# Kernel tuning notes

Hardware: AMD Instinct MI355X
Metric: run time of the kernel (lower is better)

The kernel has to match this reference:

```python
import jax, jax.numpy as jnp
import numpy as np

N_NODES = 50000
N_EDGES = 640000
D = 128
N_RELS = 16
N_NTYPES = 8


def setup_inputs() -> dict:
    key = jax.random.key(0)
    ks = jax.random.split(key, 9)
    return {
        "feats": jax.random.normal(ks[0], (N_NODES, D), dtype=jnp.float32),
        "W_edge": jax.random.normal(ks[1], (N_RELS, D, D), dtype=jnp.float32) / np.sqrt(D),
        "b_edge": jax.random.normal(ks[2], (N_RELS, D), dtype=jnp.float32) * 0.02,
        "W_node": jax.random.normal(ks[3], (N_NTYPES, D, D), dtype=jnp.float32) / np.sqrt(D),
        "b_node": jax.random.normal(ks[4], (N_NTYPES, D), dtype=jnp.float32) * 0.02,
        "src": jax.random.randint(ks[5], (N_EDGES,), 0, N_NODES, dtype=jnp.int32),
        "dst": jax.random.randint(ks[6], (N_EDGES,), 0, N_NODES, dtype=jnp.int32),
        "ntypes": jax.random.randint(ks[7], (N_NODES,), 0, N_NTYPES, dtype=jnp.int32),
        "etypes": jax.random.randint(ks[8], (N_EDGES,), 0, N_RELS, dtype=jnp.int32),
    }


def reference(feats, W_edge, b_edge, W_node, b_node, src, dst, ntypes, etypes):
    N, d = feats.shape
    T = W_edge.shape[0]
    # Per-relation linear applied to all nodes once: [T, N, out]; then gather per edge.
    hW = jnp.einsum('nd,tdf->tnf', feats, W_edge) + b_edge[:, None, :]
    msg = hW[etypes, src]  # [E, out]
    # Per-(dst-node, edge-type) in-degree counts (one_hot count normalization).
    seg = dst * T + etypes  # [E]
    counts = jax.ops.segment_sum(jnp.ones(msg.shape[0], dtype=msg.dtype), seg,
                                 num_segments=N * T)  # [N*T]
    msg = msg / counts[seg][:, None]
    # Scatter-sum messages into destination nodes (zero for isolated nodes).
    agg = jax.ops.segment_sum(msg, dst, num_segments=N)  # [N, out]
    # Type-conditional node transform + residual message + activation.
    hN = jnp.einsum('nd,tdf->tnf', feats, W_node) + b_node[:, None, :]  # [Tn, N, out]
    out = hN[ntypes, jnp.arange(N)] + agg
    return jax.nn.relu(out)
```

## Files before the change

kernel.cpp:

```cpp
#include <hip/hip_runtime.h>
#include <hip/hip_bf16.h>
#include <stdint.h>


#define D 128
#define TRELS 16
#define NTYPES 8

typedef __bf16 bf16x8 __attribute__((ext_vector_type(8)));
typedef float f32x4 __attribute__((ext_vector_type(4)));
typedef unsigned int u32x4 __attribute__((ext_vector_type(4)));

__device__ __forceinline__ unsigned short f2bf(float f) {
  union { float f; unsigned u; } v; v.f = f;
  unsigned u = v.u;
  return (unsigned short)((u + 0x7FFFu + ((u >> 16) & 1u)) >> 16);
}
__device__ __forceinline__ float bf2f(unsigned short h) {
  union { unsigned u; float f; } v; v.u = ((unsigned)h) << 16;
  return v.f;
}
__device__ __forceinline__ void bfpair(unsigned u, float& lo, float& hi) {
  union { unsigned u; float f; } a, b;
  a.u = u << 16; b.u = u & 0xffff0000u;
  lo = a.f; hi = b.f;
}

__global__ void prep_k(const float* __restrict__ feats,
                       const float* __restrict__ We,
                       const float* __restrict__ Wn,
                       unsigned short* __restrict__ featsbf,
                       unsigned short* __restrict__ WeT,
                       unsigned short* __restrict__ WnT,
                       int nfeat) {
  int idx = blockIdx.x * 256 + threadIdx.x;
  if (idx < nfeat) { featsbf[idx] = f2bf(feats[idx]); return; }
  idx -= nfeat;
  if (idx < TRELS * D * D) {
    int t = idx >> 14, rem = idx & 16383;
    int n = rem >> 7, k = rem & 127;
    WeT[idx] = f2bf(We[t * 16384 + k * 128 + n]);
    return;
  }
  idx -= TRELS * D * D;
  if (idx < NTYPES * D * D) {
    int t = idx >> 14, rem = idx & 16383;
    int n = rem >> 7, k = rem & 127;
    WnT[idx] = f2bf(Wn[t * 16384 + k * 128 + n]);
  }
}

__global__ void hist_k(const int* __restrict__ dst, const int* __restrict__ etypes,
                       const int* __restrict__ ntypes, int E, int N,
                       int* __restrict__ cnt, int* __restrict__ nhist) {
  __shared__ int sh_n[NTYPES];
  int tid = threadIdx.x;
  if (tid < NTYPES) sh_n[tid] = 0;
  __syncthreads();
  int g = blockIdx.x * 256 + tid;
  if (g < E) atomicAdd(&cnt[dst[g] * TRELS + etypes[g]], 1);
  if (g < N) atomicAdd(&sh_n[ntypes[g]], 1);
  __syncthreads();
  if (tid < NTYPES && sh_n[tid]) atomicAdd(&nhist[tid], sh_n[tid]);
}

__global__ void scan1_k(const int* __restrict__ cnt, int* __restrict__ doff,
                        int* __restrict__ bsum, int N) {
  __shared__ int sd[256];
  int b = blockIdx.x, tid = threadIdx.x;
  int base = b * 1024 + tid * 4;
  int v[4]; int tot = 0;
  for (int j = 0; j < 4; ++j) {
    int i = base + j;
    int dg = 0;
    if (i < N) {
      const int* row = cnt + i * TRELS;
#pragma unroll
      for (int et = 0; et < TRELS; ++et) dg += row[et];
    }
    v[j] = tot; tot += dg;
  }
  sd[tid] = tot;
  __syncthreads();
  for (int off = 1; off < 256; off <<= 1) {
    int t = (tid >= off) ? sd[tid - off] : 0;
    __syncthreads();
    sd[tid] += t;
    __syncthreads();
  }
  int excl = sd[tid] - tot;
  for (int j = 0; j < 4; ++j) {
    int i = base + j;
    if (i < N) doff[i] = excl + v[j];
  }
  if (tid == 255) bsum[b] = sd[255];
}

__global__ void scan2_k(int* __restrict__ misc, int* __restrict__ bsum, int nb) {
  if (threadIdx.x != 0) return;
  int run = 0;
  for (int b = 0; b < nb; ++b) { int t = bsum[b]; bsum[b] = run; run += t; }
  int* noff = misc; int* ntb = misc + 9; int* ncur = misc + 18; int* nhist = misc + 26;
  int s = 0, ts = 0;
  for (int t = 0; t < NTYPES; ++t) {
    noff[t] = s; ncur[t] = s; ntb[t] = ts;
    s += nhist[t]; ts += (nhist[t] + 127) >> 7;
  }
  noff[NTYPES] = s; ntb[NTYPES] = ts;
}

__global__ void scan3_k(int* __restrict__ doff, int* __restrict__ dcur,
                        const int* __restrict__ bsum, int N, int E) {
  int b = blockIdx.x, tid = threadIdx.x;
  int add = bsum[b];
  int base = b * 1024 + tid * 4;
  for (int j = 0; j < 4; ++j) {
    int i = base + j;
    if (i < N) { int o = doff[i] + add; doff[i] = o; dcur[i] = o; }
  }
  if (b == 0 && tid == 0) doff[N] = E;
}

__global__ void scatter_k(const int* __restrict__ src, const int* __restrict__ dst,
                          const int* __restrict__ etypes, const int* __restrict__ ntypes,
                          int E, int N, int* __restrict__ misc,
                          int* __restrict__ dcur,
                          int* __restrict__ edst, int* __restrict__ nsorted) {
  __shared__ int lc_n[NTYPES], lb_n[NTYPES];
  int tid = threadIdx.x;
  if (tid < NTYPES) lc_n[tid] = 0;
  __syncthreads();
  int g = blockIdx.x * 256 + tid;
  if (g < E) {
    int d = dst[g];
    int pos = atomicAdd(&dcur[d], 1);
    edst[pos] = src[g] * TRELS + etypes[g];
  }
  int tn = -1, idn = 0;
  if (g < N) { tn = ntypes[g]; idn = atomicAdd(&lc_n[tn], 1); }
  __syncthreads();
  if (tid < NTYPES && lc_n[tid]) lb_n[tid] = atomicAdd(&misc[18 + tid], lc_n[tid]);
  __syncthreads();
  if (g < N) nsorted[lb_n[tn] + idn] = g;
}

__global__ __launch_bounds__(256) void hw_gemm_k(
    const unsigned short* __restrict__ featsbf,
    const unsigned short* __restrict__ WeT,
    unsigned short* __restrict__ hW, int N, int mtiles) {
  __shared__ unsigned char Asm[128 * 264];
  int tid = threadIdx.x;

  int G = mtiles * 16;
  int q = G >> 3, rmod = G & 7;
  int xcd = blockIdx.x & 7, bidx = blockIdx.x >> 3;
  int wrk = (xcd < rmod) ? (xcd * (q + 1) + bidx)
                         : (rmod * (q + 1) + (xcd - rmod) * q + bidx);
  int tile = wrk >> 4;
  int et = wrk & 15;

  int lane = tid & 63, w = tid >> 6;
  int m = lane & 15, qd = lane >> 4;
  int rw = (w & 1) * 64, cw = (w >> 1) * 64;

  const unsigned short* WB = WeT + et * (D * D);
  bf16x8 bfr[4][4];
#pragma unroll
  for (int ks = 0; ks < 4; ++ks)
#pragma unroll
    for (int j = 0; j < 4; ++j)
      bfr[ks][j] = *reinterpret_cast<const bf16x8*>(WB + (cw + j * 16 + m) * D + ks * 32 + qd * 8);

  int r = tid >> 1, h = tid & 1;
  int row = tile * 128 + r;
  if (row < N) {
    const u32x4* gp = reinterpret_cast<const u32x4*>(featsbf + (size_t)row * D);
#pragma unroll
    for (int cc = 0; cc < 8; ++cc) {
      int c = h * 8 + cc;
      *reinterpret_cast<u32x4*>(&Asm[r * 256 + ((c ^ (r & 7)) << 4)]) = gp[c];
    }
  }
  __syncthreads();

  f32x4 acc[4][4];
#pragma unroll
  for (int i = 0; i < 4; ++i)
#pragma unroll
    for (int j = 0; j < 4; ++j) acc[i][j] = (f32x4){0.f, 0.f, 0.f, 0.f};

#pragma unroll
  for (int ks = 0; ks < 4; ++ks) {
    bf16x8 a[4];
#pragma unroll
    for (int i = 0; i < 4; ++i) {
      int rr = rw + i * 16 + m;
      int c = ks * 4 + qd;
      a[i] = *reinterpret_cast<const bf16x8*>(&Asm[rr * 256 + ((c ^ (rr & 7)) << 4)]);
    }
#pragma unroll
    for (int i = 0; i < 4; ++i)
#pragma unroll
      for (int j = 0; j < 4; ++j)
        acc[i][j] = __builtin_amdgcn_mfma_f32_16x16x32_bf16(a[i], bfr[ks][j], acc[i][j], 0, 0, 0);
  }

  __syncthreads();
  unsigned short* Cs = reinterpret_cast<unsigned short*>(Asm);
#pragma unroll
  for (int i = 0; i < 4; ++i)
#pragma unroll
    for (int j = 0; j < 4; ++j)
#pragma unroll
      for (int reg = 0; reg < 4; ++reg) {
        int rr = rw + i * 16 + qd * 4 + reg;
        Cs[rr * 132 + cw + j * 16 + m] = f2bf(acc[i][j][reg]);
      }
  __syncthreads();
  char* gout = (char*)(hW + ((size_t)et * N + (size_t)tile * 128) * D);
#pragma unroll
  for (int cp = 0; cp < 8; ++cp) {
    int o = cp * 4096 + tid * 16;
    int rloc = o >> 8;
    if (tile * 128 + rloc < N) {
      u32x4 v = *reinterpret_cast<const u32x4*>(&Asm[rloc * 264 + (o & 255)]);
      __builtin_nontemporal_store(v, reinterpret_cast<u32x4*>(gout + o));
    }
  }
}

__global__ __launch_bounds__(256) void agg_k(
    const unsigned short* __restrict__ hW,
    const float* __restrict__ b_edge,
    const int* __restrict__ cnt,
    const int* __restrict__ doff, const int* __restrict__ edst,
    float* __restrict__ agg, int N) {
  int tid = threadIdx.x;
  int lane = tid & 63, w = tid >> 6;
  int d = blockIdx.x * 4 + w;
  if (d >= N) return;

  int cv = 0;
  if (lane < TRELS) cv = cnt[d * TRELS + lane];
  float invl = (cv > 0) ? 1.0f / (float)cv : 0.0f;

  int g = lane >> 4;
  int sub = lane & 15;

  int start = doff[d], end = doff[d + 1];
  float acc[8];
#pragma unroll
  for (int z = 0; z < 8; ++z) acc[z] = 0.f;

  for (int base = start; base < end; base += 64) {
    int key = 0;
    if (base + lane < end) key = edst[base + lane];
    int nchunk = end - base; if (nchunk > 64) nchunk = 64;
#pragma unroll 2
    for (int j = 0; j < nchunk; j += 4) {
      int rr = j + g;
      int k = __shfl(key, rr, 64);
      float inv = __shfl(invl, k & 15, 64);
      if (rr < nchunk) {
        const unsigned short* hp =
            hW + ((size_t)(k & 15) * N + (size_t)(k >> 4)) * D + sub * 8;
        u32x4 hv = *reinterpret_cast<const u32x4*>(hp);
        float lo, hi;
        bfpair(hv.x, lo, hi); acc[0] += inv * lo; acc[1] += inv * hi;
        bfpair(hv.y, lo, hi); acc[2] += inv * lo; acc[3] += inv * hi;
        bfpair(hv.z, lo, hi); acc[4] += inv * lo; acc[5] += inv * hi;
        bfpair(hv.w, lo, hi); acc[6] += inv * lo; acc[7] += inv * hi;
      }
    }
  }

#pragma unroll
  for (int z = 0; z < 8; ++z) {
    acc[z] += __shfl_xor(acc[z], 16, 64);
    acc[z] += __shfl_xor(acc[z], 32, 64);
  }

  int cb = sub * 8 + (g & 1) * 4;
  f32x4 res = { acc[(g & 1) * 4 + 0], acc[(g & 1) * 4 + 1],
                acc[(g & 1) * 4 + 2], acc[(g & 1) * 4 + 3] };
#pragma unroll
  for (int et = 0; et < TRELS; ++et) {
    int c = __shfl(cv, et, 64);
    if (c > 0) {
      f32x4 b4 = *reinterpret_cast<const f32x4*>(b_edge + et * D + cb);
#pragma unroll
      for (int z = 0; z < 4; ++z) res[z] += b4[z];
    }
  }
  if (g < 2)
    *reinterpret_cast<f32x4*>(agg + (size_t)d * D + cb) = res;
}

__global__ __launch_bounds__(256) void node_gemm_k(
    const unsigned short* __restrict__ featsbf,
    const unsigned short* __restrict__ WnT,
    const float* __restrict__ b_node,
    const int* __restrict__ nsorted, const int* __restrict__ misc,
    const float* __restrict__ agg,
    float* __restrict__ out) {
  __shared__ unsigned char Asm[128 * 264];
  __shared__ int sm_node[128];
  __shared__ int s_ntb[9];
  int tid = threadIdx.x;
  if (tid < 9) s_ntb[tid] = misc[9 + tid];
  __syncthreads();
  int bid = blockIdx.x;
  if (bid >= s_ntb[8]) return;
  int t = 0;
  while (bid >= s_ntb[t + 1]) ++t;
  int tile = bid - s_ntb[t];
  int noff_t = misc[t];
  int cntT = misc[t + 1] - noff_t;

  int lane = tid & 63, w = tid >> 6;
  int m = lane & 15, q = lane >> 4;
  int rw = (w & 1) * 64, cw = (w >> 1) * 64;

  const unsigned short* WB = WnT + t * (D * D);
  bf16x8 bfr[4][4];
#pragma unroll
  for (int ks = 0; ks < 4; ++ks)
#pragma unroll
    for (int j = 0; j < 4; ++j)
      bfr[ks][j] = *reinterpret_cast<const bf16x8*>(WB + (cw + j * 16 + m) * D + ks * 32 + q * 8);

  int r = tid >> 1, h = tid & 1;
  int gidx = tile * 128 + r;
  bool rv = gidx < cntT;
  int node = 0;
  if (rv) node = nsorted[noff_t + gidx];
  if (h == 0) sm_node[r] = rv ? node : -1;
  if (rv) {
    const u32x4* gp = reinterpret_cast<const u32x4*>(featsbf + (size_t)node * D);
#pragma unroll
    for (int cc = 0; cc < 8; ++cc) {
      int c = h * 8 + cc;
      *reinterpret_cast<u32x4*>(&Asm[r * 256 + ((c ^ (r & 7)) << 4)]) = gp[c];
    }
  }
  __syncthreads();

  f32x4 acc[4][4];
#pragma unroll
  for (int i = 0; i < 4; ++i)
#pragma unroll
    for (int j = 0; j < 4; ++j) acc[i][j] = (f32x4){0.f, 0.f, 0.f, 0.f};

#pragma unroll
  for (int ks = 0; ks < 4; ++ks) {
    bf16x8 a[4];
#pragma unroll
    for (int i = 0; i < 4; ++i) {
      int rr = rw + i * 16 + m;
      int c = ks * 4 + q;
      a[i] = *reinterpret_cast<const bf16x8*>(&Asm[rr * 256 + ((c ^ (rr & 7)) << 4)]);
    }
#pragma unroll
    for (int i = 0; i < 4; ++i)
#pragma unroll
      for (int j = 0; j < 4; ++j)
        acc[i][j] = __builtin_amdgcn_mfma_f32_16x16x32_bf16(a[i], bfr[ks][j], acc[i][j], 0, 0, 0);
  }

  const float* bnp = b_node + t * D;
  float* Cf = reinterpret_cast<float*>(Asm);
  __syncthreads();
#pragma unroll
  for (int half = 0; half < 2; ++half) {
    if ((w & 1) == half) {
#pragma unroll
      for (int i = 0; i < 4; ++i)
#pragma unroll
        for (int j = 0; j < 4; ++j)
#pragma unroll
          for (int reg = 0; reg < 4; ++reg) {
            int rl = i * 16 + q * 4 + reg;
            Cf[rl * 132 + cw + j * 16 + m] = acc[i][j][reg];
          }
    }
    __syncthreads();
#pragma unroll
    for (int cp = 0; cp < 8; ++cp) {
      int o = cp * 4096 + tid * 16;
      int rl = o >> 9;
      int nd = sm_node[half * 64 + rl];
      if (nd >= 0) {
        int col = (o & 511) >> 2;
        f32x4 c = *reinterpret_cast<const f32x4*>((char*)Cf + rl * 528 + (o & 511));
        f32x4 a = *reinterpret_cast<const f32x4*>(agg + (size_t)nd * D + col);
        f32x4 b4 = *reinterpret_cast<const f32x4*>(bnp + col);
        f32x4 res;
#pragma unroll
        for (int z = 0; z < 4; ++z) res[z] = fmaxf(c[z] + a[z] + b4[z], 0.f);
        *reinterpret_cast<f32x4*>(out + (size_t)nd * D + col) = res;
      }
    }
    __syncthreads();
  }
}

static inline size_t align256(size_t x) { return (x + 255) & ~(size_t)255; }

extern "C" void kernel_launch(void* const* d_in, const int* in_sizes, int n_in,
                              void* d_out, int out_size, void* d_ws, size_t ws_size,
                              hipStream_t stream) {
  const float* feats  = (const float*)d_in[0];
  const float* W_edge = (const float*)d_in[1];
  const float* b_edge = (const float*)d_in[2];
  const float* W_node = (const float*)d_in[3];
  const float* b_node = (const float*)d_in[4];
  const int* src    = (const int*)d_in[5];
  const int* dst    = (const int*)d_in[6];
  const int* ntypes = (const int*)d_in[7];
  const int* etypes = (const int*)d_in[8];
  int N = in_sizes[0] / D;
  int E = in_sizes[5];

  char* ws = (char*)d_ws;
  size_t o_cnt  = 0;
  size_t o_misc = align256(o_cnt + (size_t)N * TRELS * 4);
  size_t zend   = align256(o_misc + 512);
  size_t o_doff = zend;
  size_t o_dcur = align256(o_doff + (size_t)(N + 1) * 4);
  size_t o_edst = align256(o_dcur + (size_t)N * 4);
  size_t o_ns   = align256(o_edst + (size_t)E * 4);
  size_t o_fb   = align256(o_ns + (size_t)N * 4);
  size_t o_we   = align256(o_fb + (size_t)N * D * 2);
  size_t o_wn   = align256(o_we + (size_t)TRELS * D * D * 2);
  size_t o_agg  = align256(o_wn + (size_t)NTYPES * D * D * 2);
  size_t o_hw   = align256(o_agg + (size_t)N * D * 4);

  int* cnt = (int*)(ws + o_cnt);
  int* misc = (int*)(ws + o_misc);
  int* doff = (int*)(ws + o_doff);
  int* dcur = (int*)(ws + o_dcur);
  int* edst = (int*)(ws + o_edst);
  int* nsorted = (int*)(ws + o_ns);
  unsigned short* featsbf = (unsigned short*)(ws + o_fb);
  unsigned short* WeT = (unsigned short*)(ws + o_we);
  unsigned short* WnT = (unsigned short*)(ws + o_wn);
  float* agg = (float*)(ws + o_agg);
  unsigned short* hW = (unsigned short*)(ws + o_hw);
  int* bsum = misc + 64;

  (void)hipMemsetAsync(ws, 0, zend, stream);

  int nfeat = N * D;
  int ptot = nfeat + TRELS * D * D + NTYPES * D * D;
  prep_k<<<(ptot + 255) / 256, 256, 0, stream>>>(feats, W_edge, W_node, featsbf, WeT, WnT, nfeat);

  int hgrid = ((E > N ? E : N) + 255) / 256;
  hist_k<<<hgrid, 256, 0, stream>>>(dst, etypes, ntypes, E, N, cnt, misc + 26);

  int nb = (N + 1023) / 1024;
  scan1_k<<<nb, 256, 0, stream>>>(cnt, doff, bsum, N);
  scan2_k<<<1, 64, 0, stream>>>(misc, bsum, nb);
  scan3_k<<<nb, 256, 0, stream>>>(doff, dcur, bsum, N, E);

  scatter_k<<<hgrid, 256, 0, stream>>>(src, dst, etypes, ntypes, E, N, misc, dcur, edst, nsorted);

  int mtiles = (N + 127) / 128;
  hw_gemm_k<<<mtiles * 16, 256, 0, stream>>>(featsbf, WeT, hW, N, mtiles);

  agg_k<<<(N + 3) / 4, 256, 0, stream>>>(hW, b_edge, cnt, doff, edst, agg, N);

  int ngrid = mtiles + NTYPES;
  node_gemm_k<<<ngrid, 256, 0, stream>>>(featsbf, WnT, b_node, nsorted, misc, agg, (float*)d_out);
}
```

Before: 347.4 us.

## Reuse staged feature tile across four relations per block in hW GEMM

Each hW GEMM block now loads its 128-row feature tile into LDS once and computes four relation outputs, so the grid shrinks by four and A-tile reloads are amortised. The next relation's weights are prefetched into registers while the current output is written back through a separate 64-row LDS staging buffer in two halves, and a launch bound of 3 blocks per SM is added. Nontemporal stores become plain stores. In exchange there are more barriers per block, higher register pressure, and fewer blocks to spread across the GPU.

New measurement: 359.3 us. 3.4% more time.

```diff
diff --git a/kernel.cpp b/kernel.cpp
--- a/kernel.cpp
+++ b/kernel.cpp
@@ -6,6 +6,7 @@
 #define D 128
 #define TRELS 16
 #define NTYPES 8
+#define ETC 4
 
 typedef __bf16 bf16x8 __attribute__((ext_vector_type(8)));
 typedef float f32x4 __attribute__((ext_vector_type(4)));
@@ -144,32 +145,25 @@
   if (g < N) nsorted[lb_n[tn] + idn] = g;
 }
 
-__global__ __launch_bounds__(256) void hw_gemm_k(
+__global__ __launch_bounds__(256, 3) void hw_gemm_k(
     const unsigned short* __restrict__ featsbf,
     const unsigned short* __restrict__ WeT,
     unsigned short* __restrict__ hW, int N, int mtiles) {
   __shared__ unsigned char Asm[128 * 264];
+  __shared__ unsigned char Csm[64 * 264];
   int tid = threadIdx.x;
 
-  int G = mtiles * 16;
+  int G = mtiles * (TRELS / ETC);
   int q = G >> 3, rmod = G & 7;
   int xcd = blockIdx.x & 7, bidx = blockIdx.x >> 3;
   int wrk = (xcd < rmod) ? (xcd * (q + 1) + bidx)
                          : (rmod * (q + 1) + (xcd - rmod) * q + bidx);
-  int tile = wrk >> 4;
-  int et = wrk & 15;
+  int tile = wrk >> 2;
+  int etbase = (wrk & 3) * ETC;
 
   int lane = tid & 63, w = tid >> 6;
   int m = lane & 15, qd = lane >> 4;
   int rw = (w & 1) * 64, cw = (w >> 1) * 64;
-
-  const unsigned short* WB = WeT + et * (D * D);
-  bf16x8 bfr[4][4];
-#pragma unroll
-  for (int ks = 0; ks < 4; ++ks)
-#pragma unroll
-    for (int j = 0; j < 4; ++j)
-      bfr[ks][j] = *reinterpret_cast<const bf16x8*>(WB + (cw + j * 16 + m) * D + ks * 32 + qd * 8);
 
   int r = tid >> 1, h = tid & 1;
   int row = tile * 128 + r;
@@ -181,50 +175,79 @@
       *reinterpret_cast<u32x4*>(&Asm[r * 256 + ((c ^ (r & 7)) << 4)]) = gp[c];
     }
   }
-  __syncthreads();
-
-  f32x4 acc[4][4];
-#pragma unroll
-  for (int i = 0; i < 4; ++i)
-#pragma unroll
-    for (int j = 0; j < 4; ++j) acc[i][j] = (f32x4){0.f, 0.f, 0.f, 0.f};
-
-#pragma unroll
-  for (int ks = 0; ks < 4; ++ks) {
-    bf16x8 a[4];
-#pragma unroll
-    for (int i = 0; i < 4; ++i) {
-      int rr = rw + i * 16 + m;
-      int c = ks * 4 + qd;
-      a[i] = *reinterpret_cast<const bf16x8*>(&Asm[rr * 256 + ((c ^ (rr & 7)) << 4)]);
-    }
+
+  bf16x8 bfr[4][4];
+  {
+    const unsigned short* WB = WeT + (size_t)etbase * (D * D);
+#pragma unroll
+    for (int ks = 0; ks < 4; ++ks)
+#pragma unroll
+      for (int j = 0; j < 4; ++j)
+        bfr[ks][j] = *reinterpret_cast<const bf16x8*>(WB + (cw + j * 16 + m) * D + ks * 32 + qd * 8);
+  }
+  __syncthreads();
+
+#pragma unroll
+  for (int e = 0; e < ETC; ++e) {
+    int et = etbase + e;
+
+    f32x4 acc[4][4];
 #pragma unroll
     for (int i = 0; i < 4; ++i)
 #pragma unroll
-      for (int j = 0; j < 4; ++j)
-        acc[i][j] = __builtin_amdgcn_mfma_f32_16x16x32_bf16(a[i], bfr[ks][j], acc[i][j], 0, 0, 0);
-  }
-
-  __syncthreads();
-  unsigned short* Cs = reinterpret_cast<unsigned short*>(Asm);
-#pragma unroll
-  for (int i = 0; i < 4; ++i)
-#pragma unroll
-    for (int j = 0; j < 4; ++j)
-#pragma unroll
-      for (int reg = 0; reg < 4; ++reg) {
-        int rr = rw + i * 16 + qd * 4 + reg;
-        Cs[rr * 132 + cw + j * 16 + m] = f2bf(acc[i][j][reg]);
+      for (int j = 0; j < 4; ++j) acc[i][j] = (f32x4){0.f, 0.f, 0.f, 0.f};
+
+#pragma unroll
+    for (int ks = 0; ks < 4; ++ks) {
+      bf16x8 a[4];
+#pragma unroll
+      for (int i = 0; i < 4; ++i) {
+        int rr = rw + i * 16 + m;
+        int c = ks * 4 + qd;
+        a[i] = *reinterpret_cast<const bf16x8*>(&Asm[rr * 256 + ((c ^ (rr & 7)) << 4)]);
       }
-  __syncthreads();
-  char* gout = (char*)(hW + ((size_t)et * N + (size_t)tile * 128) * D);
-#pragma unroll
-  for (int cp = 0; cp < 8; ++cp) {
-    int o = cp * 4096 + tid * 16;
-    int rloc = o >> 8;
-    if (tile * 128 + rloc < N) {
-      u32x4 v = *reinterpret_cast<const u32x4*>(&Asm[rloc * 264 + (o & 255)]);
-      __builtin_nontemporal_store(v, reinterpret_cast<u32x4*>(gout + o));
+#pragma unroll
+      for (int i = 0; i < 4; ++i)
+#pragma unroll
+        for (int j = 0; j < 4; ++j)
+          acc[i][j] = __builtin_amdgcn_mfma_f32_16x16x32_bf16(a[i], bfr[ks][j], acc[i][j], 0, 0, 0);
+    }
+
+    if (e + 1 < ETC) {
+      const unsigned short* WB = WeT + (size_t)(et + 1) * (D * D);
+#pragma unroll
+      for (int ks = 0; ks < 4; ++ks)
+#pragma unroll
+        for (int j = 0; j < 4; ++j)
+          bfr[ks][j] = *reinterpret_cast<const bf16x8*>(WB + (cw + j * 16 + m) * D + ks * 32 + qd * 8);
+    }
+
+    char* gout = (char*)(hW + ((size_t)et * N + (size_t)tile * 128) * D);
+    unsigned short* Cs = reinterpret_cast<unsigned short*>(Csm);
+#pragma unroll
+    for (int half = 0; half < 2; ++half) {
+      __syncthreads();
+      if ((w & 1) == half) {
+#pragma unroll
+        for (int i = 0; i < 4; ++i)
+#pragma unroll
+          for (int j = 0; j < 4; ++j)
+#pragma unroll
+            for (int reg = 0; reg < 4; ++reg) {
+              int rl = i * 16 + qd * 4 + reg;
+              Cs[rl * 132 + cw + j * 16 + m] = f2bf(acc[i][j][reg]);
+            }
+      }
+      __syncthreads();
+#pragma unroll
+      for (int cp = 0; cp < 4; ++cp) {
+        int o = cp * 4096 + tid * 16;
+        int rloc = o >> 8;
+        if (tile * 128 + half * 64 + rloc < N) {
+          u32x4 v = *reinterpret_cast<const u32x4*>(&Csm[rloc * 264 + (o & 255)]);
+          *reinterpret_cast<u32x4*>(gout + half * 16384 + o) = v;
+        }
+      }
     }
   }
 }
@@ -465,7 +488,7 @@
   scatter_k<<<hgrid, 256, 0, stream>>>(src, dst, etypes, ntypes, E, N, misc, dcur, edst, nsorted);
 
   int mtiles = (N + 127) / 128;
-  hw_gemm_k<<<mtiles * 16, 256, 0, stream>>>(featsbf, WeT, hW, N, mtiles);
+  hw_gemm_k<<<mtiles * (TRELS / ETC), 256, 0, stream>>>(featsbf, WeT, hW, N, mtiles);
 
   agg_k<<<(N + 3) / 4, 256, 0, stream>>>(hW, b_edge, cnt, doff, edst, agg, N);
 
```

## Split edge-relation GEMM and aggregation into two half-relation passes for cache residency

Applied to the files above, without the earlier changes.

Splits the per-relation transform into two passes of 8 relations each, with each pass writing a half-size hW buffer (about 100MB bf16 instead of 200MB) and then running aggregation over only the edges of those relations. The second aggregation pass adds its result into agg. Stores are switched from nontemporal to regular so the half buffer can stay resident in the large last-level cache for the gather. The cost is two extra launches, a second pass over the edge lists and a read-modify-write of agg.

Measured after the change: 367.0 us. 1.06x slower.

```diff
diff --git a/kernel.cpp b/kernel.cpp
--- a/kernel.cpp
+++ b/kernel.cpp
@@ -6,6 +6,7 @@
 #define D 128
 #define TRELS 16
 #define NTYPES 8
+#define ETPH 8
 
 typedef __bf16 bf16x8 __attribute__((ext_vector_type(8)));
 typedef float f32x4 __attribute__((ext_vector_type(4)));
@@ -147,23 +148,23 @@
 __global__ __launch_bounds__(256) void hw_gemm_k(
     const unsigned short* __restrict__ featsbf,
     const unsigned short* __restrict__ WeT,
-    unsigned short* __restrict__ hW, int N, int mtiles) {
+    unsigned short* __restrict__ hWp, int N, int mtiles, int etoff) {
   __shared__ unsigned char Asm[128 * 264];
   int tid = threadIdx.x;
 
-  int G = mtiles * 16;
+  int G = mtiles * ETPH;
   int q = G >> 3, rmod = G & 7;
   int xcd = blockIdx.x & 7, bidx = blockIdx.x >> 3;
   int wrk = (xcd < rmod) ? (xcd * (q + 1) + bidx)
                          : (rmod * (q + 1) + (xcd - rmod) * q + bidx);
-  int tile = wrk >> 4;
-  int et = wrk & 15;
+  int tile = wrk >> 3;
+  int etl = wrk & 7;
 
   int lane = tid & 63, w = tid >> 6;
   int m = lane & 15, qd = lane >> 4;
   int rw = (w & 1) * 64, cw = (w >> 1) * 64;
 
-  const unsigned short* WB = WeT + et * (D * D);
+  const unsigned short* WB = WeT + (size_t)(etoff + etl) * (D * D);
   bf16x8 bfr[4][4];
 #pragma unroll
   for (int ks = 0; ks < 4; ++ks)
@@ -217,24 +218,24 @@
         Cs[rr * 132 + cw + j * 16 + m] = f2bf(acc[i][j][reg]);
       }
   __syncthreads();
-  char* gout = (char*)(hW + ((size_t)et * N + (size_t)tile * 128) * D);
+  char* gout = (char*)(hWp + ((size_t)etl * N + (size_t)tile * 128) * D);
 #pragma unroll
   for (int cp = 0; cp < 8; ++cp) {
     int o = cp * 4096 + tid * 16;
     int rloc = o >> 8;
     if (tile * 128 + rloc < N) {
       u32x4 v = *reinterpret_cast<const u32x4*>(&Asm[rloc * 264 + (o & 255)]);
-      __builtin_nontemporal_store(v, reinterpret_cast<u32x4*>(gout + o));
+      *reinterpret_cast<u32x4*>(gout + o) = v;
     }
   }
 }
 
 __global__ __launch_bounds__(256) void agg_k(
-    const unsigned short* __restrict__ hW,
+    const unsigned short* __restrict__ hWp,
     const float* __restrict__ b_edge,
     const int* __restrict__ cnt,
     const int* __restrict__ doff, const int* __restrict__ edst,
-    float* __restrict__ agg, int N) {
+    float* __restrict__ agg, int N, int etoff, int pass) {
   int tid = threadIdx.x;
   int lane = tid & 63, w = tid >> 6;
   int d = blockIdx.x * 4 + w;
@@ -261,9 +262,10 @@
       int rr = j + g;
       int k = __shfl(key, rr, 64);
       float inv = __shfl(invl, k & 15, 64);
-      if (rr < nchunk) {
+      unsigned etl = (unsigned)((k & 15) - etoff);
+      if (rr < nchunk && etl < (unsigned)ETPH) {
         const unsigned short* hp =
-            hW + ((size_t)(k & 15) * N + (size_t)(k >> 4)) * D + sub * 8;
+            hWp + ((size_t)etl * N + (size_t)(k >> 4)) * D + sub * 8;
         u32x4 hv = *reinterpret_cast<const u32x4*>(hp);
         float lo, hi;
         bfpair(hv.x, lo, hi); acc[0] += inv * lo; acc[1] += inv * hi;
@@ -283,17 +285,26 @@
   int cb = sub * 8 + (g & 1) * 4;
   f32x4 res = { acc[(g & 1) * 4 + 0], acc[(g & 1) * 4 + 1],
                 acc[(g & 1) * 4 + 2], acc[(g & 1) * 4 + 3] };
-#pragma unroll
-  for (int et = 0; et < TRELS; ++et) {
-    int c = __shfl(cv, et, 64);
-    if (c > 0) {
-      f32x4 b4 = *reinterpret_cast<const f32x4*>(b_edge + et * D + cb);
-#pragma unroll
-      for (int z = 0; z < 4; ++z) res[z] += b4[z];
-    }
-  }
-  if (g < 2)
-    *reinterpret_cast<f32x4*>(agg + (size_t)d * D + cb) = res;
+  if (pass == 0) {
+#pragma unroll
+    for (int et = 0; et < TRELS; ++et) {
+      int c = __shfl(cv, et, 64);
+      if (c > 0) {
+        f32x4 b4 = *reinterpret_cast<const f32x4*>(b_edge + et * D + cb);
+#pragma unroll
+        for (int z = 0; z < 4; ++z) res[z] += b4[z];
+      }
+    }
+  }
+  if (g < 2) {
+    f32x4* op = reinterpret_cast<f32x4*>(agg + (size_t)d * D + cb);
+    if (pass) {
+      f32x4 old = *op;
+#pragma unroll
+      for (int z = 0; z < 4; ++z) res[z] += old[z];
+    }
+    *op = res;
+  }
 }
 
 __global__ __launch_bounds__(256) void node_gemm_k(
@@ -465,9 +476,11 @@
   scatter_k<<<hgrid, 256, 0, stream>>>(src, dst, etypes, ntypes, E, N, misc, dcur, edst, nsorted);
 
   int mtiles = (N + 127) / 128;
-  hw_gemm_k<<<mtiles * 16, 256, 0, stream>>>(featsbf, WeT, hW, N, mtiles);
-
-  agg_k<<<(N + 3) / 4, 256, 0, stream>>>(hW, b_edge, cnt, doff, edst, agg, N);
+  int agrid = (N + 3) / 4;
+  hw_gemm_k<<<mtiles * ETPH, 256, 0, stream>>>(featsbf, WeT, hW, N, mtiles, 0);
+  agg_k<<<agrid, 256, 0, stream>>>(hW, b_edge, cnt, doff, edst, agg, N, 0, 0);
+  hw_gemm_k<<<mtiles * ETPH, 256, 0, stream>>>(featsbf, WeT, hW, N, mtiles, 8);
+  agg_k<<<agrid, 256, 0, stream>>>(hW, b_edge, cnt, doff, edst, agg, N, 8, 1);
 
   int ngrid = mtiles + NTYPES;
   node_gemm_k<<<ngrid, 256, 0, stream>>>(featsbf, WnT, b_node, nsorted, misc, agg, (float*)d_out);
```

## Fuse per-relation aggregation before transform, eliminating the hW intermediate

Applied to the files above, without the earlier changes.

Sorts edges by (dst, relation) bucket and, per 64-destination tile, averages raw bf16 source features per relation, then multiplies by each relation's weight with MFMA and accumulates. Bias is added once per nonempty relation. This avoids materialising and re-reading the large per-relation transformed feature tensor. In exchange, the scan grows to N×16 entries, and the fused kernel serialises edge gathers per thread with many block barriers. Precision also changes, since averaged features are rounded to bf16 before the GEMM.

Measured after the change: 462.0 us. +33.0%, slower.

```diff
diff --git a/kernel.cpp b/kernel.cpp
--- a/kernel.cpp
+++ b/kernel.cpp
@@ -6,6 +6,7 @@
 #define D 128
 #define TRELS 16
 #define NTYPES 8
+#define DSTB 64
 
 typedef __bf16 bf16x8 __attribute__((ext_vector_type(8)));
 typedef float f32x4 __attribute__((ext_vector_type(4)));
@@ -15,10 +16,6 @@
   union { float f; unsigned u; } v; v.f = f;
   unsigned u = v.u;
   return (unsigned short)((u + 0x7FFFu + ((u >> 16) & 1u)) >> 16);
-}
-__device__ __forceinline__ float bf2f(unsigned short h) {
-  union { unsigned u; float f; } v; v.u = ((unsigned)h) << 16;
-  return v.f;
 }
 __device__ __forceinline__ void bfpair(unsigned u, float& lo, float& hi) {
   union { unsigned u; float f; } a, b;
@@ -64,21 +61,16 @@
   if (tid < NTYPES && sh_n[tid]) atomicAdd(&nhist[tid], sh_n[tid]);
 }
 
-__global__ void scan1_k(const int* __restrict__ cnt, int* __restrict__ doff,
-                        int* __restrict__ bsum, int N) {
+__global__ void scan1_k(const int* __restrict__ cnt, int* __restrict__ poff,
+                        int* __restrict__ bsum, int M) {
   __shared__ int sd[256];
   int b = blockIdx.x, tid = threadIdx.x;
   int base = b * 1024 + tid * 4;
   int v[4]; int tot = 0;
   for (int j = 0; j < 4; ++j) {
     int i = base + j;
-    int dg = 0;
-    if (i < N) {
-      const int* row = cnt + i * TRELS;
-#pragma unroll
-      for (int et = 0; et < TRELS; ++et) dg += row[et];
-    }
-    v[j] = tot; tot += dg;
+    int c = (i < M) ? cnt[i] : 0;
+    v[j] = tot; tot += c;
   }
   sd[tid] = tot;
   __syncthreads();
@@ -91,7 +83,7 @@
   int excl = sd[tid] - tot;
   for (int j = 0; j < 4; ++j) {
     int i = base + j;
-    if (i < N) doff[i] = excl + v[j];
+    if (i < M) poff[i] = excl + v[j];
   }
   if (tid == 255) bsum[b] = sd[255];
 }
@@ -109,32 +101,32 @@
   noff[NTYPES] = s; ntb[NTYPES] = ts;
 }
 
-__global__ void scan3_k(int* __restrict__ doff, int* __restrict__ dcur,
-                        const int* __restrict__ bsum, int N, int E) {
+__global__ void scan3_k(int* __restrict__ poff, int* __restrict__ pcur,
+                        const int* __restrict__ bsum, int M, int E) {
   int b = blockIdx.x, tid = threadIdx.x;
   int add = bsum[b];
   int base = b * 1024 + tid * 4;
   for (int j = 0; j < 4; ++j) {
     int i = base + j;
-    if (i < N) { int o = doff[i] + add; doff[i] = o; dcur[i] = o; }
-  }
-  if (b == 0 && tid == 0) doff[N] = E;
+    if (i < M) { int o = poff[i] + add; poff[i] = o; pcur[i] = o; }
+  }
+  if (b == 0 && tid == 0) poff[M] = E;
 }
 
 __global__ void scatter_k(const int* __restrict__ src, const int* __restrict__ dst,
                           const int* __restrict__ etypes, const int* __restrict__ ntypes,
                           int E, int N, int* __restrict__ misc,
-                          int* __restrict__ dcur,
-                          int* __restrict__ edst, int* __restrict__ nsorted) {
+                          int* __restrict__ pcur,
+                          int* __restrict__ esrc, int* __restrict__ nsorted) {
   __shared__ int lc_n[NTYPES], lb_n[NTYPES];
   int tid = threadIdx.x;
   if (tid < NTYPES) lc_n[tid] = 0;
   __syncthreads();
   int g = blockIdx.x * 256 + tid;
   if (g < E) {
-    int d = dst[g];
-    int pos = atomicAdd(&dcur[d], 1);
-    edst[pos] = src[g] * TRELS + etypes[g];
+    int key = dst[g] * TRELS + etypes[g];
+    int pos = atomicAdd(&pcur[key], 1);
+    esrc[pos] = src[g];
   }
   int tn = -1, idn = 0;
   if (g < N) { tn = ntypes[g]; idn = atomicAdd(&lc_n[tn], 1); }
@@ -144,156 +136,136 @@
   if (g < N) nsorted[lb_n[tn] + idn] = g;
 }
 
-__global__ __launch_bounds__(256) void hw_gemm_k(
+__global__ __launch_bounds__(256, 3) void fused_k(
     const unsigned short* __restrict__ featsbf,
     const unsigned short* __restrict__ WeT,
-    unsigned short* __restrict__ hW, int N, int mtiles) {
-  __shared__ unsigned char Asm[128 * 264];
+    const float* __restrict__ b_edge,
+    const int* __restrict__ poff, const int* __restrict__ esrc,
+    float* __restrict__ agg, int N) {
+  __shared__ unsigned char Asm[DSTB * 264];
+  __shared__ int spoff[DSTB * TRELS + 1];
+  __shared__ unsigned short smask[DSTB];
   int tid = threadIdx.x;
-
-  int G = mtiles * 16;
-  int q = G >> 3, rmod = G & 7;
-  int xcd = blockIdx.x & 7, bidx = blockIdx.x >> 3;
-  int wrk = (xcd < rmod) ? (xcd * (q + 1) + bidx)
-                         : (rmod * (q + 1) + (xcd - rmod) * q + bidx);
-  int tile = wrk >> 4;
-  int et = wrk & 15;
-
+  int tile = blockIdx.x;
   int lane = tid & 63, w = tid >> 6;
   int m = lane & 15, qd = lane >> 4;
-  int rw = (w & 1) * 64, cw = (w >> 1) * 64;
-
-  const unsigned short* WB = WeT + et * (D * D);
-  bf16x8 bfr[4][4];
-#pragma unroll
-  for (int ks = 0; ks < 4; ++ks)
-#pragma unroll
-    for (int j = 0; j < 4; ++j)
-      bfr[ks][j] = *reinterpret_cast<const bf16x8*>(WB + (cw + j * 16 + m) * D + ks * 32 + qd * 8);
-
-  int r = tid >> 1, h = tid & 1;
-  int row = tile * 128 + r;
-  if (row < N) {
-    const u32x4* gp = reinterpret_cast<const u32x4*>(featsbf + (size_t)row * D);
-#pragma unroll
-    for (int cc = 0; cc < 8; ++cc) {
-      int c = h * 8 + cc;
-      *reinterpret_cast<u32x4*>(&Asm[r * 256 + ((c ^ (r & 7)) << 4)]) = gp[c];
-    }
-  }
-  __syncthreads();
-
-  f32x4 acc[4][4];
-#pragma unroll
-  for (int i = 0; i < 4; ++i)
+  int rw = (w & 1) * 32, cw = (w >> 1) * 64;
+
+  int M = N * TRELS;
+  for (int i = tid; i < DSTB * TRELS + 1; i += 256) {
+    int g = tile * (DSTB * TRELS) + i;
+    spoff[i] = (g <= M) ? poff[g] : poff[M];
+  }
+  __syncthreads();
+
+  int r = tid >> 2, cg = tid & 3;
+  unsigned mask = 0;
+
+  f32x4 acc[2][4];
+#pragma unroll
+  for (int i = 0; i < 2; ++i)
 #pragma unroll
     for (int j = 0; j < 4; ++j) acc[i][j] = (f32x4){0.f, 0.f, 0.f, 0.f};
 
-#pragma unroll
-  for (int ks = 0; ks < 4; ++ks) {
-    bf16x8 a[4];
-#pragma unroll
-    for (int i = 0; i < 4; ++i) {
-      int rr = rw + i * 16 + m;
-      int c = ks * 4 + qd;
-      a[i] = *reinterpret_cast<const bf16x8*>(&Asm[rr * 256 + ((c ^ (rr & 7)) << 4)]);
-    }
-#pragma unroll
-    for (int i = 0; i < 4; ++i)
+  for (int et = 0; et < TRELS; ++et) {
+    int s0 = spoff[r * TRELS + et];
+    int s1 = spoff[r * TRELS + et + 1];
+    float fa[32];
+#pragma unroll
+    for (int z = 0; z < 32; ++z) fa[z] = 0.f;
+    for (int e = s0; e < s1; ++e) {
+      int sn = esrc[e];
+      const u32x4* fp = reinterpret_cast<const u32x4*>(featsbf + (size_t)sn * D + cg * 32);
+      u32x4 vv[4];
+#pragma unroll
+      for (int t = 0; t < 4; ++t) vv[t] = fp[t];
+#pragma unroll
+      for (int t = 0; t < 4; ++t)
+#pragma unroll
+        for (int z = 0; z < 4; ++z) {
+          float lo, hi;
+          bfpair(vv[t][z], lo, hi);
+          fa[t * 8 + z * 2] += lo; fa[t * 8 + z * 2 + 1] += hi;
+        }
+    }
+    int c = s1 - s0;
+    float inv = (c > 0) ? 1.0f / (float)c : 0.0f;
+    if (c > 0) mask |= (1u << et);
+#pragma unroll
+    for (int cc = 0; cc < 4; ++cc) {
+      u32x4 pk;
+#pragma unroll
+      for (int z = 0; z < 4; ++z) {
+        unsigned l0 = f2bf(fa[cc * 8 + z * 2] * inv);
+        unsigned h0 = f2bf(fa[cc * 8 + z * 2 + 1] * inv);
+        pk[z] = l0 | (h0 << 16);
+      }
+      int cu = cg * 4 + cc;
+      *reinterpret_cast<u32x4*>(&Asm[r * 256 + ((cu ^ (r & 7)) << 4)]) = pk;
+    }
+    const unsigned short* WB = WeT + (size_t)et * (D * D);
+    bf16x8 bfr[4][4];
+#pragma unroll
+    for (int ks = 0; ks < 4; ++ks)
 #pragma unroll
       for (int j = 0; j < 4; ++j)
-        acc[i][j] = __builtin_amdgcn_mfma_f32_16x16x32_bf16(a[i], bfr[ks][j], acc[i][j], 0, 0, 0);
-  }
-
-  __syncthreads();
-  unsigned short* Cs = reinterpret_cast<unsigned short*>(Asm);
-#pragma unroll
-  for (int i = 0; i < 4; ++i)
-#pragma unroll
-    for (int j = 0; j < 4; ++j)
-#pragma unroll
-      for (int reg = 0; reg < 4; ++reg) {
-        int rr = rw + i * 16 + qd * 4 + reg;
-        Cs[rr * 132 + cw + j * 16 + m] = f2bf(acc[i][j][reg]);
+        bfr[ks][j] = *reinterpret_cast<const bf16x8*>(WB + (cw + j * 16 + m) * D + ks * 32 + qd * 8);
+    __syncthreads();
+#pragma unroll
+    for (int ks = 0; ks < 4; ++ks) {
+      bf16x8 a[2];
+#pragma unroll
+      for (int i = 0; i < 2; ++i) {
+        int rr = rw + i * 16 + m;
+        int cu = ks * 4 + qd;
+        a[i] = *reinterpret_cast<const bf16x8*>(&Asm[rr * 256 + ((cu ^ (rr & 7)) << 4)]);
       }
-  __syncthreads();
-  char* gout = (char*)(hW + ((size_t)et * N + (size_t)tile * 128) * D);
-#pragma unroll
-  for (int cp = 0; cp < 8; ++cp) {
-    int o = cp * 4096 + tid * 16;
-    int rloc = o >> 8;
-    if (tile * 128 + rloc < N) {
-      u32x4 v = *reinterpret_cast<const u32x4*>(&Asm[rloc * 264 + (o & 255)]);
-      __builtin_nontemporal_store(v, reinterpret_cast<u32x4*>(gout + o));
-    }
-  }
-}
-
-__global__ __launch_bounds__(256) void agg_k(
-    const unsigned short* __restrict__ hW,
-    const float* __restrict__ b_edge,
-    const int* __restrict__ cnt,
-    const int* __restrict__ doff, const int* __restrict__ edst,
-    float* __restrict__ agg, int N) {
-  int tid = threadIdx.x;
-  int lane = tid & 63, w = tid >> 6;
-  int d = blockIdx.x * 4 + w;
-  if (d >= N) return;
-
-  int cv = 0;
-  if (lane < TRELS) cv = cnt[d * TRELS + lane];
-  float invl = (cv > 0) ? 1.0f / (float)cv : 0.0f;
-
-  int g = lane >> 4;
-  int sub = lane & 15;
-
-  int start = doff[d], end = doff[d + 1];
-  float acc[8];
-#pragma unroll
-  for (int z = 0; z < 8; ++z) acc[z] = 0.f;
-
-  for (int base = start; base < end; base += 64) {
-    int key = 0;
-    if (base + lane < end) key = edst[base + lane];
-    int nchunk = end - base; if (nchunk > 64) nchunk = 64;
-#pragma unroll 2
-    for (int j = 0; j < nchunk; j += 4) {
-      int rr = j + g;
-      int k = __shfl(key, rr, 64);
-      float inv = __shfl(invl, k & 15, 64);
-      if (rr < nchunk) {
-        const unsigned short* hp =
-            hW + ((size_t)(k & 15) * N + (size_t)(k >> 4)) * D + sub * 8;
-        u32x4 hv = *reinterpret_cast<const u32x4*>(hp);
-        float lo, hi;
-        bfpair(hv.x, lo, hi); acc[0] += inv * lo; acc[1] += inv * hi;
-        bfpair(hv.y, lo, hi); acc[2] += inv * lo; acc[3] += inv * hi;
-        bfpair(hv.z, lo, hi); acc[4] += inv * lo; acc[5] += inv * hi;
-        bfpair(hv.w, lo, hi); acc[6] += inv * lo; acc[7] += inv * hi;
+#pragma unroll
+      for (int i = 0; i < 2; ++i)
+#pragma unroll
+        for (int j = 0; j < 4; ++j)
+          acc[i][j] = __builtin_amdgcn_mfma_f32_16x16x32_bf16(a[i], bfr[ks][j], acc[i][j], 0, 0, 0);
+    }
+    __syncthreads();
+  }
+
+  if (cg == 0) smask[r] = (unsigned short)mask;
+
+  float* Cf = reinterpret_cast<float*>(Asm);
+#pragma unroll
+  for (int half = 0; half < 2; ++half) {
+    __syncthreads();
+    if ((w & 1) == half) {
+#pragma unroll
+      for (int i = 0; i < 2; ++i)
+#pragma unroll
+        for (int j = 0; j < 4; ++j)
+#pragma unroll
+          for (int reg = 0; reg < 4; ++reg) {
+            int rl = i * 16 + qd * 4 + reg;
+            Cf[rl * 132 + cw + j * 16 + m] = acc[i][j][reg];
+          }
+    }
+    __syncthreads();
+#pragma unroll
+    for (int cp = 0; cp < 4; ++cp) {
+      int o = cp * 4096 + tid * 16;
+      int rl = o >> 9;
+      int dd = tile * DSTB + half * 32 + rl;
+      if (dd < N) {
+        int col = (o & 511) >> 2;
+        f32x4 cv = *reinterpret_cast<const f32x4*>((char*)Cf + rl * 528 + (o & 511));
+        unsigned mk = smask[half * 32 + rl];
+        while (mk) {
+          int et = __builtin_ctz(mk); mk &= mk - 1;
+          f32x4 b4 = *reinterpret_cast<const f32x4*>(b_edge + et * D + col);
+#pragma unroll
+          for (int z = 0; z < 4; ++z) cv[z] += b4[z];
+        }
+        *reinterpret_cast<f32x4*>(agg + (size_t)dd * D + col) = cv;
       }
     }
   }
-
-#pragma unroll
-  for (int z = 0; z < 8; ++z) {
-    acc[z] += __shfl_xor(acc[z], 16, 64);
-    acc[z] += __shfl_xor(acc[z], 32, 64);
-  }
-
-  int cb = sub * 8 + (g & 1) * 4;
-  f32x4 res = { acc[(g & 1) * 4 + 0], acc[(g & 1) * 4 + 1],
-                acc[(g & 1) * 4 + 2], acc[(g & 1) * 4 + 3] };
-#pragma unroll
-  for (int et = 0; et < TRELS; ++et) {
-    int c = __shfl(cv, et, 64);
-    if (c > 0) {
-      f32x4 b4 = *reinterpret_cast<const f32x4*>(b_edge + et * D + cb);
-#pragma unroll
-      for (int z = 0; z < 4; ++z) res[z] += b4[z];
-    }
-  }
-  if (g < 2)
-    *reinterpret_cast<f32x4*>(agg + (size_t)d * D + cb) = res;
 }
 
 __global__ __launch_bounds__(256) void node_gemm_k(
@@ -420,33 +392,33 @@
   const int* etypes = (const int*)d_in[8];
   int N = in_sizes[0] / D;
   int E = in_sizes[5];
+  int M = N * TRELS;
 
   char* ws = (char*)d_ws;
   size_t o_cnt  = 0;
-  size_t o_misc = align256(o_cnt + (size_t)N * TRELS * 4);
+  size_t o_misc = align256(o_cnt + (size_t)M * 4);
   size_t zend   = align256(o_misc + 512);
-  size_t o_doff = zend;
-  size_t o_dcur = align256(o_doff + (size_t)(N + 1) * 4);
-  size_t o_edst = align256(o_dcur + (size_t)N * 4);
-  size_t o_ns   = align256(o_edst + (size_t)E * 4);
+  size_t o_poff = zend;
+  size_t o_pcur = align256(o_poff + (size_t)(M + 1) * 4);
+  size_t o_bsum = align256(o_pcur + (size_t)M * 4);
+  size_t o_esrc = align256(o_bsum + 4096);
+  size_t o_ns   = align256(o_esrc + (size_t)E * 4);
   size_t o_fb   = align256(o_ns + (size_t)N * 4);
   size_t o_we   = align256(o_fb + (size_t)N * D * 2);
   size_t o_wn   = align256(o_we + (size_t)TRELS * D * D * 2);
   size_t o_agg  = align256(o_wn + (size_t)NTYPES * D * D * 2);
-  size_t o_hw   = align256(o_agg + (size_t)N * D * 4);
 
   int* cnt = (int*)(ws + o_cnt);
   int* misc = (int*)(ws + o_misc);
-  int* doff = (int*)(ws + o_doff);
-  int* dcur = (int*)(ws + o_dcur);
-  int* edst = (int*)(ws + o_edst);
+  int* poff = (int*)(ws + o_poff);
+  int* pcur = (int*)(ws + o_pcur);
+  int* bsum = (int*)(ws + o_bsum);
+  int* esrc = (int*)(ws + o_esrc);
   int* nsorted = (int*)(ws + o_ns);
   unsigned short* featsbf = (unsigned short*)(ws + o_fb);
   unsigned short* WeT = (unsigned short*)(ws + o_we);
   unsigned short* WnT = (unsigned short*)(ws + o_wn);
   float* agg = (float*)(ws + o_agg);
-  unsigned short* hW = (unsigned short*)(ws + o_hw);
-  int* bsum = misc + 64;
 
   (void)hipMemsetAsync(ws, 0, zend, stream);
 
@@ -457,18 +429,17 @@
   int hgrid = ((E > N ? E : N) + 255) / 256;
   hist_k<<<hgrid, 256, 0, stream>>>(dst, etypes, ntypes, E, N, cnt, misc + 26);
 
-  int nb = (N + 1023) / 1024;
-  scan1_k<<<nb, 256, 0, stream>>>(cnt, doff, bsum, N);
+  int nb = (M + 1023) / 1024;
+  scan1_k<<<nb, 256, 0, stream>>>(cnt, poff, bsum, M);
   scan2_k<<<1, 64, 0, stream>>>(misc, bsum, nb);
-  scan3_k<<<nb, 256, 0, stream>>>(doff, dcur, bsum, N, E);
-
-  scatter_k<<<hgrid, 256, 0, stream>>>(src, dst, etypes, ntypes, E, N, misc, dcur, edst, nsorted);
+  scan3_k<<<nb, 256, 0, stream>>>(poff, pcur, bsum, M, E);
+
+  scatter_k<<<hgrid, 256, 0, stream>>>(src, dst, etypes, ntypes, E, N, misc, pcur, esrc, nsorted);
+
+  int fgrid = (N + DSTB - 1) / DSTB;
+  fused_k<<<fgrid, 256, 0, stream>>>(featsbf, WeT, b_edge, poff, esrc, agg, N);
 
   int mtiles = (N + 127) / 128;
-  hw_gemm_k<<<mtiles * 16, 256, 0, stream>>>(featsbf, WeT, hW, N, mtiles);
-
-  agg_k<<<(N + 3) / 4, 256, 0, stream>>>(hW, b_edge, cnt, doff, edst, agg, N);
-
   int ngrid = mtiles + NTYPES;
   node_gemm_k<<<ngrid, 256, 0, stream>>>(featsbf, WnT, b_node, nsorted, misc, agg, (float*)d_out);
 }
```
